# Optimization experiments

Measured on AMD Instinct MI355X. Metric: run time of the kernel, lower is better.

The kernel has to match this reference:

```python
import jax, jax.numpy as jnp
import numpy as np

_CH = [(3,64),(64,64),(64,128),(128,128),(128,256),(256,256),(256,256),(256,512),(512,512),(512,512),(512,512),(512,512),(512,512)]
_RES = [32,32,16,16,8,8,8,4,4,4,2,2,2]
# (conv index, pool index applied after, or None)
_PLAN = [(0,None),(1,0),(2,None),(3,1),(4,None),(5,None),(6,2),(7,None),(8,None),(9,3),(10,None),(11,None),(12,4)]


def _bilinear(x, py, px):
    # x: [B,C,H,W]; py/px: [B,K2,H,W] float sampling coords (zero-padded outside)
    B, C, H, W = x.shape
    y0 = jnp.floor(py); x0 = jnp.floor(px)
    wy1 = (py - y0)[:, None]  # [B,1,K2,H,W]
    wx1 = (px - x0)[:, None]
    xf = x.reshape(B, C, H * W)

    def gather(yi, xi):
        valid = ((yi >= 0) & (yi < H) & (xi >= 0) & (xi < W)).astype(x.dtype)
        idx = (jnp.clip(yi, 0, H - 1) * W + jnp.clip(xi, 0, W - 1)).astype(jnp.int32)
        def gb(xb, ib, vb):
            return xb[:, ib.reshape(-1)].reshape((xb.shape[0],) + ib.shape) * vb[None]
        return jax.vmap(gb)(xf, idx, valid)  # [B,C,K2,H,W]

    g00 = gather(y0, x0); g01 = gather(y0, x0 + 1)
    g10 = gather(y0 + 1, x0); g11 = gather(y0 + 1, x0 + 1)
    return (g00 * (1 - wy1) * (1 - wx1) + g01 * (1 - wy1) * wx1
            + g10 * wy1 * (1 - wx1) + g11 * wy1 * wx1)


def _deform_conv(x, offset, w, b):
    # torchvision-style DeformConv2d, stride 1, padding 1, 3x3 kernel
    B, C, H, W = x.shape
    K = w.shape[-1]
    off = offset.reshape(B, K * K, 2, H, W)  # per kernel tap: (dy, dx)
    kk = jnp.arange(K, dtype=x.dtype) - (K // 2)
    ky = jnp.repeat(kk, K); kx = jnp.tile(kk, K)  # [K2]
    py = jnp.arange(H, dtype=x.dtype)[None, None, :, None] + ky[None, :, None, None] + off[:, :, 0]
    px = jnp.arange(W, dtype=x.dtype)[None, None, None, :] + kx[None, :, None, None] + off[:, :, 1]
    s = _bilinear(x, py, px)  # [B,C,K2,H,W]
    out = jnp.einsum('bckhw,ock->bohw', s, w.reshape(w.shape[0], C, K * K))
    return out + b[None, :, None, None]


def _bn_relu(x, g, beta):
    # training-mode BatchNorm2d (batch statistics, eps=1e-5) + ReLU
    m = jnp.mean(x, axis=(0, 2, 3), keepdims=True)
    v = jnp.mean((x - m) ** 2, axis=(0, 2, 3), keepdims=True)
    xn = (x - m) * jax.lax.rsqrt(v + 1e-5)
    return jax.nn.relu(xn * g[None, :, None, None] + beta[None, :, None, None])


def _deform_pool(x, perm, new_perm):
    # permutation-indexed 2x2 max pool: gather by perm, pool, re-permute output
    B, C, H, W = x.shape
    xp = x.reshape(B, C, H * W)[:, :, perm].reshape(B, C, H, W)
    p = xp.reshape(B, C, H // 2, 2, W // 2, 2).max(axis=(3, 5))
    return p.reshape(B, C, (H // 2) * (W // 2))[:, :, new_perm].reshape(B, C, H // 2, W // 2)


def _forward(x, offs, ws, bs, gs, betas, perms, nperms, fws, fbs):
    for ci, pi in _PLAN:
        x = _deform_conv(x, offs[ci], ws[ci], bs[ci])
        x = _bn_relu(x, gs[ci], betas[ci])
        if pi is not None:
            x = _deform_pool(x, perms[pi], nperms[pi])
    h = x.reshape(x.shape[0], -1)  # [B,512]
    h = jax.nn.relu(h @ fws[0].T + fbs[0])
    h = jax.nn.relu(h @ fws[1].T + fbs[1])
    return h @ fws[2].T + fbs[2]


def setup_inputs() -> dict:
    key = jax.random.key(0)
    ks = iter(jax.random.split(key, 128))
    B = 32
    d = {"x": jax.random.normal(next(ks), (B, 3, 32, 32), jnp.float32)}
    for i, ((ci, co), r) in enumerate(zip(_CH, _RES), 1):
        d[f"off{i}"] = jax.random.normal(next(ks), (B, 18, r, r), jnp.float32) * 0.5
        d[f"w{i}"] = jax.random.normal(next(ks), (co, ci, 3, 3), jnp.float32) * (1.0 / np.sqrt(ci * 9))
        d[f"b{i}"] = jnp.zeros((co,), jnp.float32)
        d[f"g{i}"] = jnp.ones((co,), jnp.float32)
        d[f"bb{i}"] = jnp.zeros((co,), jnp.float32)
    for i, r in enumerate([32, 16, 8, 4, 2], 1):
        d[f"perm{i}"] = jax.random.permutation(next(ks), r * r)
        d[f"nperm{i}"] = jax.random.permutation(next(ks), (r // 2) * (r // 2))
    for i, (di, do) in enumerate([(512, 4096), (4096, 4096), (4096, 100)], 1):
        d[f"fw{i}"] = jax.random.normal(next(ks), (do, di), jnp.float32) * (1.0 / np.sqrt(di))
        d[f"fb{i}"] = jnp.zeros((do,), jnp.float32)
    return d


def reference(x,
              off1, off2, off3, off4, off5, off6, off7, off8, off9, off10, off11, off12, off13,
              w1, w2, w3, w4, w5, w6, w7, w8, w9, w10, w11, w12, w13,
              b1, b2, b3, b4, b5, b6, b7, b8, b9, b10, b11, b12, b13,
              g1, g2, g3, g4, g5, g6, g7, g8, g9, g10, g11, g12, g13,
              bb1, bb2, bb3, bb4, bb5, bb6, bb7, bb8, bb9, bb10, bb11, bb12, bb13,
              perm1, perm2, perm3, perm4, perm5,
              nperm1, nperm2, nperm3, nperm4, nperm5,
              fw1, fb1, fw2, fb2, fw3, fb3):
    offs = [off1, off2, off3, off4, off5, off6, off7, off8, off9, off10, off11, off12, off13]
    ws = [w1, w2, w3, w4, w5, w6, w7, w8, w9, w10, w11, w12, w13]
    bs = [b1, b2, b3, b4, b5, b6, b7, b8, b9, b10, b11, b12, b13]
    gs = [g1, g2, g3, g4, g5, g6, g7, g8, g9, g10, g11, g12, g13]
    betas = [bb1, bb2, bb3, bb4, bb5, bb6, bb7, bb8, bb9, bb10, bb11, bb12, bb13]
    perms = [perm1, perm2, perm3, perm4, perm5]
    nperms = [nperm1, nperm2, nperm3, nperm4, nperm5]
    return _forward(x, offs, ws, bs, gs, betas, perms, nperms, [fw1, fw2, fw3], [fb1, fb2, fb3])
```

## Files before the change

kernel.cpp:

```cpp
#include <hip/hip_runtime.h>
#include <hip/hip_bf16.h>

typedef __hip_bfloat16 bf16;
typedef __attribute__((ext_vector_type(8))) short short8;
typedef __attribute__((ext_vector_type(4))) short short4v;
typedef __attribute__((ext_vector_type(4))) float f32x4;
typedef unsigned short u16;
#define BF2F(x) __bfloat162float(x)

__device__ __forceinline__ u16 f2bfbits(float v) {
  bf16 h = __float2bfloat16(v);
  return *(u16*)&h;
}
__device__ __forceinline__ float bfbits2f(u16 u) {
  bf16 h; *(u16*)&h = u;
  return BF2F(h);
}
__device__ __forceinline__ void splitbf(float v, u16& hi, u16& lo) {
  hi = f2bfbits(v);
  lo = f2bfbits(v - bfbits2f(hi));
}

union VecU {
  u16 u[8];
  short8 s;
};

__global__ void nchw2nhwc_kernel(const float* __restrict__ in, float* __restrict__ out,
                                 int B, int C, int HW) {
  int i = blockIdx.x * blockDim.x + threadIdx.x;
  int total = B * C * HW;
  if (i >= total) return;
  int c = i % C; int p = (i / C) % HW; int b = i / (C * HW);
  out[i] = in[((size_t)b * C + c) * HW + p];
}

template<int C, int Kp>
__device__ __forceinline__ void wtc_pair(const float* __restrict__ w, u16* __restrict__ Wh,
// ... 20 lines not shown
    const float* w4, const float* w5, const float* w6, const float* w7,
    const float* w8, const float* w9, const float* w10, const float* w11,
    const float* w12, u16* __restrict__ Wh, u16* __restrict__ Wl) {
  int i = blockIdx.x * blockDim.x + threadIdx.x;
  if (i >= PAIR_TOTAL + PAD_TOTAL) return;
  if (i >= PAIR_TOTAL) {
    int t = i - PAIR_TOTAL;
    int co = t / 5, k = 27 + t % 5;
    int o = co * 32 + k;
    Wh[o] = 0; Wl[o] = 0;
    return;
  }
  if      (i < 192)     wtc_pair<3, 32>(w0, Wh + 0, Wl + 0, i);
  else if (i < 4288)    wtc_pair<64, 576>(w1, Wh + 2048, Wl + 2048, i - 192);
  else if (i < 12480)   wtc_pair<64, 576>(w2, Wh + 38912, Wl + 38912, i - 4288);
  else if (i < 28864)   wtc_pair<128, 1152>(w3, Wh + 112640, Wl + 112640, i - 12480);
  else if (i < 61632)   wtc_pair<128, 1152>(w4, Wh + 260096, Wl + 260096, i - 28864);
  else if (i < 127168)  wtc_pair<256, 2304>(w5, Wh + 555008, Wl + 555008, i - 61632);
  else if (i < 192704)  wtc_pair<256, 2304>(w6, Wh + 1144832, Wl + 1144832, i - 127168);
  else if (i < 323776)  wtc_pair<256, 2304>(w7, Wh + 1734656, Wl + 1734656, i - 192704);
  else if (i < 585920)  wtc_pair<512, 4608>(w8, Wh + 2914304, Wl + 2914304, i - 323776);
  else if (i < 848064)  wtc_pair<512, 4608>(w9, Wh + 5273600, Wl + 5273600, i - 585920);
  else if (i < 1110208) wtc_pair<512, 4608>(w10, Wh + 7632896, Wl + 7632896, i - 848064);
  else if (i < 1372352) wtc_pair<512, 4608>(w11, Wh + 9992192, Wl + 9992192, i - 1110208);
  else                  wtc_pair<512, 4608>(w12, Wh + 12351488, Wl + 12351488, i - 1372352);
}

__global__ void act_convert(const float* __restrict__ x,
                            u16* __restrict__ Ah, u16* __restrict__ Al, int total) {
  int i = blockIdx.x * blockDim.x + threadIdx.x;
  if (i >= total) return;
  u16 hh, ll; splitbf(x[i], hh, ll);
  Ah[i] = hh; Al[i] = ll;
}

__global__ __launch_bounds__(256) void deform_sample_v3(
    const float* __restrict__ act, const float* __restrict__ stp, int bnmode,
    const float* __restrict__ off, u16* __restrict__ Sh, u16* __restrict__ Sl,
    int m0, int Mc, int B, int H, int W, int C, int Kp) {
  int i = blockIdx.x * blockDim.x + threadIdx.x;
  int c8n = C >> 3;
  int total = Mc * 9 * c8n;
  if (i >= total) return;
  int c8 = i % c8n;
  int t = i / c8n;
  int k2 = t % 9;
  int ml = t / 9;
  int m = m0 + ml;
  int HW = H * W;
  int b = m / HW; int p = m - b * HW; int y = p / W; int x = p - y * W;
  size_t ob = (size_t)b * 18 * HW + p;
  float dy = off[ob + (size_t)(2 * k2) * HW];
  float dx = off[ob + (size_t)(2 * k2 + 1) * HW];
  float py = (float)(y + k2 / 3 - 1) + dy;
  float px = (float)(x + k2 % 3 - 1) + dx;
  float y0f = floorf(py), x0f = floorf(px);
  float wy = py - y0f, wx = px - x0f;
  int iy0 = (int)y0f, ix0 = (int)x0f;
  int iy1 = iy0 + 1, ix1 = ix0 + 1;
  float w00 = (1.f - wy) * (1.f - wx), w01 = (1.f - wy) * wx;
  float w10 = wy * (1.f - wx), w11 = wy * wx;
  if (iy0 < 0 || iy0 >= H) { w00 = 0.f; w01 = 0.f; }
  if (iy1 < 0 || iy1 >= H) { w10 = 0.f; w11 = 0.f; }
  if (ix0 < 0 || ix0 >= W) { w00 = 0.f; w10 = 0.f; }
  if (ix1 < 0 || ix1 >= W) { w01 = 0.f; w11 = 0.f; }
  int cy0 = min(max(iy0, 0), H - 1), cy1 = min(max(iy1, 0), H - 1);
  int cx0 = min(max(ix0, 0), W - 1), cx1 = min(max(ix1, 0), W - 1);
  int c = c8 << 3;
  size_t rowb = (size_t)b * HW;
  const float* p00 = act + (rowb + cy0 * W + cx0) * C + c;
  const float* p01 = act + (rowb + cy0 * W + cx1) * C + c;
  const float* p10 = act + (rowb + cy1 * W + cx0) * C + c;
  const float* p11 = act + (rowb + cy1 * W + cx1) * C + c;
  float4 a00 = *(const float4*)p00, b00 = *(const float4*)(p00 + 4);
  float4 a01 = *(const float4*)p01, b01 = *(const float4*)(p01 + 4);
  float4 a10 = *(const float4*)p10, b10 = *(const float4*)(p10 + 4);
  float4 a11 = *(const float4*)p11, b11 = *(const float4*)(p11 + 4);
  float v00[8] = {a00.x, a00.y, a00.z, a00.w, b00.x, b00.y, b00.z, b00.w};
  float v01[8] = {a01.x, a01.y, a01.z, a01.w, b01.x, b01.y, b01.z, b01.w};
  float v10[8] = {a10.x, a10.y, a10.z, a10.w, b10.x, b10.y, b10.z, b10.w};
  float v11[8] = {a11.x, a11.y, a11.z, a11.w, b11.x, b11.y, b11.z, b11.w};
  if (bnmode) {
    float4 s0 = *(const float4*)(stp + c), s1 = *(const float4*)(stp + c + 4);
    float4 h0 = *(const float4*)(stp + 512 + c), h1 = *(const float4*)(stp + 512 + c + 4);
    float sc[8] = {s0.x, s0.y, s0.z, s0.w, s1.x, s1.y, s1.z, s1.w};
    float sh[8] = {h0.x, h0.y, h0.z, h0.w, h1.x, h1.y, h1.z, h1.w};
#pragma unroll
    for (int j = 0; j < 8; ++j) {
      v00[j] = fmaxf(v00[j] * sc[j] + sh[j], 0.f);
      v01[j] = fmaxf(v01[j] * sc[j] + sh[j], 0.f);
      v10[j] = fmaxf(v10[j] * sc[j] + sh[j], 0.f);
      v11[j] = fmaxf(v11[j] * sc[j] + sh[j], 0.f);
    }
  }
  VecU uh, ul;
#pragma unroll
  for (int j = 0; j < 8; ++j) {
    float r = w00 * v00[j] + w01 * v01[j] + w10 * v10[j] + w11 * v11[j];
    splitbf(r, uh.u[j], ul.u[j]);
  }
  size_t base = (size_t)ml * Kp + (size_t)k2 * C + c;
  *(short8*)(Sh + base) = uh.s;
  *(short8*)(Sl + base) = ul.s;
}

__global__ __launch_bounds__(256) void deform_sample_scalar(
    const float* __restrict__ act, const float* __restrict__ off,
    u16* __restrict__ Sh, u16* __restrict__ Sl,
    int m0, int Mc, int B, int H, int W, int C, int Kp) {
  int i = blockIdx.x * blockDim.x + threadIdx.x;
  int total = Mc * Kp;
  if (i >= total) return;
  int kp = i % Kp;
  int ml = i / Kp;
  float val = 0.f;
  int K = 9 * C;
  if (kp < K) {
    int c = kp % C; int k2 = kp / C;
    int m = m0 + ml;
    int HW = H * W;
    int b = m / HW; int p = m - b * HW; int y = p / W; int x = p - y * W;
    size_t ob = (size_t)b * 18 * HW + p;
    float dy = off[ob + (size_t)(2 * k2) * HW];
    float dx = off[ob + (size_t)(2 * k2 + 1) * HW];
    float py = (float)(y + k2 / 3 - 1) + dy;
    float px = (float)(x + k2 % 3 - 1) + dx;
    float y0f = floorf(py), x0f = floorf(px);
    float wy = py - y0f, wx = px - x0f;
    int iy0 = (int)y0f, ix0 = (int)x0f;
    int iy1 = iy0 + 1, ix1 = ix0 + 1;
    float w00 = (1.f - wy) * (1.f - wx), w01 = (1.f - wy) * wx;
    float w10 = wy * (1.f - wx), w11 = wy * wx;
    if (iy0 < 0 || iy0 >= H) { w00 = 0.f; w01 = 0.f; }
    if (iy1 < 0 || iy1 >= H) { w10 = 0.f; w11 = 0.f; }
    if (ix0 < 0 || ix0 >= W) { w00 = 0.f; w10 = 0.f; }
    if (ix1 < 0 || ix1 >= W) { w01 = 0.f; w11 = 0.f; }
    int cy0 = min(max(iy0, 0), H - 1), cy1 = min(max(iy1, 0), H - 1);
    int cx0 = min(max(ix0, 0), W - 1), cx1 = min(max(ix1, 0), W - 1);
    size_t rowb = (size_t)b * HW;
    float v00 = act[(rowb + cy0 * W + cx0) * C + c];
    float v01 = act[(rowb + cy0 * W + cx1) * C + c];
    float v10 = act[(rowb + cy1 * W + cx0) * C + c];
    float v11 = act[(rowb + cy1 * W + cx1) * C + c];
    val = w00 * v00 + w01 * v01 + w10 * v10 + w11 * v11;
  }
  u16 hh, ll; splitbf(val, hh, ll);
  size_t base = (size_t)ml * Kp + kp;
  Sh[base] = hh; Sl[base] = ll;
}

#define LDA 40

__global__ __launch_bounds__(256) void mfma_gemm_tiled(
    const u16* __restrict__ Ah, const u16* __restrict__ Al,
    const u16* __restrict__ Bh, const u16* __restrict__ Bl,
    float* __restrict__ Cf, int M, int N, int Kp, int kPerZ, int splitMode) {
  __shared__ __align__(16) u16 lds[2 * 4 * 64 * LDA];
  const int TS = 64 * LDA;
  const int BS = 4 * TS;
  int tid = threadIdx.x;
  int lane = tid & 63, wave = tid >> 6;
  int l15 = lane & 15, quad = lane >> 4;
  int wr = wave >> 1, wc = wave & 1;
  int m0 = blockIdx.x * 64, n0 = blockIdx.y * 64;
  int kStart = blockIdx.z * kPerZ;
  int kEnd = min(Kp, kStart + kPerZ);
  int nSteps = (kEnd - kStart) >> 5;

  int sr = tid >> 2, sc = (tid & 3) << 3;
  const u16* gAh = Ah + (size_t)(m0 + sr) * Kp + kStart + sc;
  const u16* gAl = Al + (size_t)(m0 + sr) * Kp + kStart + sc;
  const u16* gBh = Bh + (size_t)(n0 + sr) * Kp + kStart + sc;
  const u16* gBl = Bl + (size_t)(n0 + sr) * Kp + kStart + sc;
  int soff = sr * LDA + sc;

  f32x4 z4 = {0.f, 0.f, 0.f, 0.f};
  f32x4 acc00 = z4, acc01 = z4, acc10 = z4, acc11 = z4;

  {
    short8 a = *(const short8*)gAh;
    short8 b = *(const short8*)gAl;
    short8 c = *(const short8*)gBh;
    short8 d = *(const short8*)gBl;
    *(short8*)&lds[0 * TS + soff] = a;
    *(short8*)&lds[1 * TS + soff] = b;
    *(short8*)&lds[2 * TS + soff] = c;
    *(short8*)&lds[3 * TS + soff] = d;
  }
  __syncthreads();

  int raoff = (wr * 32 + l15) * LDA + quad * 8;
  int rboff = (wc * 32 + l15) * LDA + quad * 8;

  for (int i = 0; i < nSteps; ++i) {
    int cb = (i & 1) * BS;
    bool hasNext = (i + 1 < nSteps);
    short8 nA, nB, nC, nD;
    if (hasNext) {
      int kn = (i + 1) << 5;
      nA = *(const short8*)(gAh + kn);
      nB = *(const short8*)(gAl + kn);
      nC = *(const short8*)(gBh + kn);
      nD = *(const short8*)(gBl + kn);
    }
    short8 ah0 = *(const short8*)&lds[cb + 0 * TS + raoff];
    short8 ah1 = *(const short8*)&lds[cb + 0 * TS + raoff + 16 * LDA];
    short8 al0 = *(const short8*)&lds[cb + 1 * TS + raoff];
    short8 al1 = *(const short8*)&lds[cb + 1 * TS + raoff + 16 * LDA];
    short8 bh0 = *(const short8*)&lds[cb + 2 * TS + rboff];
    short8 bh1 = *(const short8*)&lds[cb + 2 * TS + rboff + 16 * LDA];
    short8 bl0 = *(const short8*)&lds[cb + 3 * TS + rboff];
    short8 bl1 = *(const short8*)&lds[cb + 3 * TS + rboff + 16 * LDA];
    acc00 = __builtin_amdgcn_mfma_f32_16x16x32_bf16(ah0, bh0, acc00, 0, 0, 0);
    acc01 = __builtin_amdgcn_mfma_f32_16x16x32_bf16(ah0, bh1, acc01, 0, 0, 0);
    acc10 = __builtin_amdgcn_mfma_f32_16x16x32_bf16(ah1, bh0, acc10, 0, 0, 0);
    acc11 = __builtin_amdgcn_mfma_f32_16x16x32_bf16(ah1, bh1, acc11, 0, 0, 0);
    acc00 = __builtin_amdgcn_mfma_f32_16x16x32_bf16(ah0, bl0, acc00, 0, 0, 0);
    acc01 = __builtin_amdgcn_mfma_f32_16x16x32_bf16(ah0, bl1, acc01, 0, 0, 0);
    acc10 = __builtin_amdgcn_mfma_f32_16x16x32_bf16(ah1, bl0, acc10, 0, 0, 0);
    acc11 = __builtin_amdgcn_mfma_f32_16x16x32_bf16(ah1, bl1, acc11, 0, 0, 0);
    acc00 = __builtin_amdgcn_mfma_f32_16x16x32_bf16(al0, bh0, acc00, 0, 0, 0);
    acc01 = __builtin_amdgcn_mfma_f32_16x16x32_bf16(al0, bh1, acc01, 0, 0, 0);
    acc10 = __builtin_amdgcn_mfma_f32_16x16x32_bf16(al1, bh0, acc10, 0, 0, 0);
    acc11 = __builtin_amdgcn_mfma_f32_16x16x32_bf16(al1, bh1, acc11, 0, 0, 0);
    if (hasNext) {
      int ob = cb ^ BS;
      *(short8*)&lds[ob + 0 * TS + soff] = nA;
      *(short8*)&lds[ob + 1 * TS + soff] = nB;
      *(short8*)&lds[ob + 2 * TS + soff] = nC;
      *(short8*)&lds[ob + 3 * TS + soff] = nD;
      __syncthreads();
    }
  }

  float* out = Cf + (splitMode ? (size_t)blockIdx.z * M * N : (size_t)0);
  f32x4 av[2][2] = {{acc00, acc01}, {acc10, acc11}};
#pragma unroll
  for (int t = 0; t < 2; ++t) {
    int mB = m0 + wr * 32 + t * 16 + (quad << 2);
#pragma unroll
    for (int u = 0; u < 2; ++u) {
      int n = n0 + wc * 32 + u * 16 + l15;
      f32x4 a = av[t][u];
#pragma unroll
      for (int reg = 0; reg < 4; ++reg) {
        int m = mB + reg;
        out[(size_t)m * N + n] = a[reg];
      }
    }
  }
}

#define LDAF 40

__global__ __launch_bounds__(256) void mfma_gemm_fc4(
    const u16* __restrict__ Ah, const u16* __restrict__ Al,
    const float* __restrict__ Bw, float* __restrict__ Cf,
    int N, int K, int kPerZ) {
  __shared__ __align__(16) u16 sB[2][2][64 * LDAF];
  int tid = threadIdx.x;
  int lane = tid & 63, wave = tid >> 6;
  int l15 = lane & 15, quad = lane >> 4;
  int wm = wave >> 1, wn = wave & 1;
  int n0 = blockIdx.y * 64;
  int kStart = blockIdx.z * kPerZ;
  int kEnd = min(K, kStart + kPerZ);
  int nSteps = (kEnd - kStart) >> 5;

  int sr = tid >> 2, sc = (tid & 3) << 3;
  int gn = n0 + sr; if (gn >= N) gn = 0;
  const float* gB = Bw + (size_t)gn * K + kStart + sc;
  int soff = sr * LDAF + sc;

  const u16* pa = Ah + (size_t)(wm * 16 + l15) * K + kStart + (quad << 3);
  const u16* qa = Al + (size_t)(wm * 16 + l15) * K + kStart + (quad << 3);

  f32x4 z4 = {0.f, 0.f, 0.f, 0.f};
  f32x4 acc0 = z4, acc1 = z4;

  {
    float4 x0 = *(const float4*)gB;
    float4 x1 = *(const float4*)(gB + 4);
    float f[8] = {x0.x, x0.y, x0.z, x0.w, x1.x, x1.y, x1.z, x1.w};
    VecU uh, ul;
#pragma unroll
// ... 44 lines not shown
#pragma unroll
  for (int u = 0; u < 2; ++u) {
    int n = n0 + wn * 32 + u * 16 + l15;
    if (n >= N) continue;
    f32x4 a = av[u];
#pragma unroll
    for (int reg = 0; reg < 4; ++reg) {
      int m = wm * 16 + (quad << 2) + reg;
      out[(size_t)m * N + n] = a[reg];
    }
  }
}

__global__ void fc_reduce_convert(const float* __restrict__ P, const float* __restrict__ bias,
                                  u16* __restrict__ Ah, u16* __restrict__ Al,
                                  int MN, int N, int zs) {
  int i = blockIdx.x * blockDim.x + threadIdx.x;
  if (i >= MN) return;
  float s = 0.f;
  for (int z = 0; z < zs; ++z) s += P[(size_t)z * MN + i];
  s += bias[i % N];
  if (s < 0.f) s = 0.f;
  u16 hh, ll; splitbf(s, hh, ll);
  Ah[i] = hh; Al[i] = ll;
}

__global__ void fc_reduce_out(const float* __restrict__ P, const float* __restrict__ bias,
                              float* __restrict__ out, int MN, int N, int zs) {
  int i = blockIdx.x * blockDim.x + threadIdx.x;
  if (i >= MN) return;
  float s = 0.f;
  for (int z = 0; z < zs; ++z) s += P[(size_t)z * MN + i];
  out[i] = s + bias[i % N];
}

__global__ void zreduce_kernel(const float* __restrict__ P, float* __restrict__ out,
                               int MN, int zs) {
  int i = blockIdx.x * blockDim.x + threadIdx.x;
  if (i >= MN) return;
  float s = 0.f;
  for (int z = 0; z < zs; ++z) s += P[(size_t)z * MN + i];
  out[i] = s;
}

__global__ __launch_bounds__(256) void bn_stats_fused(
    const float* __restrict__ P, float* __restrict__ out, float* __restrict__ st,
    const float* __restrict__ g, const float* __restrict__ bb,
    int M, int C, int rowsPerBlock, int nBlocks, int zs, int writeOut) {
  __shared__ float sh[512];
  __shared__ int isLast;
  size_t MN = (size_t)M * C;
  int t = threadIdx.x;
  int r0 = blockIdx.x * rowsPerBlock;
  int r1 = min(M, r0 + rowsPerBlock);
  if (C >= 256) {
    for (int c = t; c < C; c += 256) {
      float s = 0.f, ss = 0.f;
      for (int r = r0; r < r1; ++r) {
        size_t idx = (size_t)r * C + c;
        float v = P[idx];
        for (int z = 1; z < zs; ++z) v += P[(size_t)z * MN + idx];
        if (writeOut) out[idx] = v;
        s += v; ss += v * v;
      }
      atomicAdd(&st[c], s); atomicAdd(&st[512 + c], ss);
    }
  } else {
    int rpb = 256 / C;
    int c = t % C; int ro = t / C;
    float s = 0.f, ss = 0.f;
    for (int r = r0 + ro; r < r1; r += rpb) {
      size_t idx = (size_t)r * C + c;
      float v = P[idx];
      for (int z = 1; z < zs; ++z) v += P[(size_t)z * MN + idx];
      if (writeOut) out[idx] = v;
// ... 43 lines not shown
#pragma unroll
  for (int dy = 0; dy < 2; ++dy)
#pragma unroll
    for (int dx = 0; dx < 2; ++dx) {
      int p = min(max(perm[(2 * qy + dy) * H + (2 * qx + dx)], 0), HW - 1);
      float v = in[((size_t)b * HW + p) * C + c];
      v = fmaxf(v * sc + sh, 0.f);
      m = fmaxf(m, v);
    }
  out[((size_t)b * oHW + j) * C + c] = m;
}

static inline void pick_split4(int gx, int gy, int Kp, int& zs, int& kPerZ) {
  int gxy = gx * gy;
  zs = 1;
  if (gxy < 512) {
    zs = (512 + gxy - 1) / gxy;
    int maxz = Kp / 32; if (maxz < 1) maxz = 1;
    if (zs > maxz) zs = maxz;
  }
  kPerZ = (((Kp + zs - 1) / zs) + 31) & ~31;
  zs = (Kp + kPerZ - 1) / kPerZ;
}

static inline void pick_splitFC(int gy, int K, int& zs, int& kPerZ) {
  zs = (512 + gy - 1) / gy;
  int maxz = K / 32; if (maxz < 1) maxz = 1;
  if (zs > maxz) zs = maxz;
  if (zs > 32) zs = 32;
  kPerZ = (((K + zs - 1) / zs) + 31) & ~31;
  zs = (K + kPerZ - 1) / kPerZ;
}

extern "C" void kernel_launch(void* const* d_in, const int* in_sizes, int n_in,
                              void* d_out, int out_size, void* d_ws, size_t ws_size,
                              hipStream_t stream) {
  const int Ci[13]  = {3, 64, 64, 128, 128, 256, 256, 256, 512, 512, 512, 512, 512};
  const int CoA[13] = {64, 64, 128, 128, 256, 256, 256, 512, 512, 512, 512, 512, 512};
  const int Rr[13]  = {32, 32, 16, 16, 8, 8, 8, 4, 4, 4, 2, 2, 2};
  const int poolAfter[13] = {-1, 0, -1, 1, -1, -1, 2, -1, -1, 3, -1, -1, 4};
  const size_t wOff[13] = {0, 2048, 38912, 112640, 260096, 555008, 1144832, 1734656,
                           2914304, 5273600, 7632896, 9992192, 12351488};
  const int WT_TOTAL = 14710784;
  const int B = 32;
  const int ST = 2304;

  size_t cursor = 0;
  auto alloc = [&](size_t bytes) {
    void* p = (char*)d_ws + cursor;
    cursor += (bytes + 255) & ~(size_t)255;
    return p;
  };
  float* stats = (float*)alloc((size_t)13 * ST * 4);
  u16*   fcPh  = (u16*)alloc((size_t)32 * 4096 * 2);
  u16*   fcPl  = (u16*)alloc((size_t)32 * 4096 * 2);
  float* A0    = (float*)alloc((size_t)2097152 * 4);
  float* A1    = (float*)alloc((size_t)2097152 * 4);
  u16*   WTh   = (u16*)alloc((size_t)WT_TOTAL * 2);
  u16*   WTl   = (u16*)alloc((size_t)WT_TOTAL * 2);
  float* Pbuf  = (float*)alloc((size_t)4194304 * 4);
  size_t remainBytes = (ws_size > cursor) ? (ws_size - cursor) : 0;
  size_t sElems = remainBytes / 4;
  if (sElems > (size_t)20971520) sElems = 20971520;
  if (sElems < (size_t)589824)  sElems = 589824;
  u16* Sh = (u16*)alloc(sElems * 2);
  u16* Sl = (u16*)alloc(sElems * 2);
  (void)in_sizes; (void)n_in; (void)out_size;

  hipMemsetAsync(stats, 0, (size_t)13 * ST * 4, stream);

  {
    int total = B * 3 * 1024;
    nchw2nhwc_kernel<<<(total + 255) / 256, 256, 0, stream>>>(
        (const float*)d_in[0], A0, B, 3, 1024);
  }
  wtc_all_v2<<<(PAIR_TOTAL + PAD_TOTAL + 255) / 256, 256, 0, stream>>>(
      (const float*)d_in[2],  (const float*)d_in[7],  (const float*)d_in[12],
      (const float*)d_in[17], (const float*)d_in[22], (const float*)d_in[27],
      (const float*)d_in[32], (const float*)d_in[37], (const float*)d_in[42],
      (const float*)d_in[47], (const float*)d_in[52], (const float*)d_in[57],
      (const float*)d_in[62], WTh, WTl);

  float* cur = A0;
  float* oth = A1;
  int needBN = 0;
  float* stp = nullptr;

  for (int l = 0; l < 13; ++l) {
    int C = Ci[l], N = CoA[l], H = Rr[l];
    int M = B * H * H, K = 9 * C, Kp = (K + 31) & ~31;
    const float* offp = (const float*)d_in[1 + l * 5 + 0];
    const float* gp   = (const float*)d_in[1 + l * 5 + 3];
    const float* bbp  = (const float*)d_in[1 + l * 5 + 4];
    float* st = stats + (size_t)l * ST;

    int MC = (int)((sElems / (size_t)Kp) & ~(size_t)63);
    if (MC < 64) MC = 64;
    if (MC > M) MC = M;
    bool singleChunk = (MC >= M);
    int lastZs = 1;
    for (int r0 = 0; r0 < M; r0 += MC) {
      int Mc = min(MC, M - r0);
      if ((C & 7) == 0) {
        int work = Mc * 9 * (C >> 3);
        deform_sample_v3<<<(work + 255) / 256, 256, 0, stream>>>(
            cur, stp, needBN, offp, Sh, Sl, r0, Mc, B, H, H, C, Kp);
      } else {
        int work = Mc * Kp;
        deform_sample_scalar<<<(work + 255) / 256, 256, 0, stream>>>(
            cur, offp, Sh, Sl, r0, Mc, B, H, H, C, Kp);
      }
      int gx = Mc / 64, gy = N / 64;
      int zs, kPerZ;
      pick_split4(gx, gy, Kp, zs, kPerZ);
      lastZs = zs;
      float* gemmOut = (zs > 1) ? Pbuf : (oth + (size_t)r0 * N);
      mfma_gemm_tiled<<<dim3(gx, gy, zs), 256, 0, stream>>>(
          Sh, Sl, WTh + wOff[l], WTl + wOff[l], gemmOut, Mc, N, Kp, kPerZ, zs > 1 ? 1 : 0);
      if (zs > 1 && !singleChunk)
        zreduce_kernel<<<(Mc * N + 255) / 256, 256, 0, stream>>>(
            Pbuf, oth + (size_t)r0 * N, Mc * N, zs);
    }

    int rowsPer = M / 128;
    if (rowsPer < 1) rowsPer = 1;
    if (rowsPer > 64) rowsPer = 64;
    int nB = (M + rowsPer - 1) / rowsPer;
    if (singleChunk && lastZs > 1)
      bn_stats_fused<<<nB, 256, 0, stream>>>(Pbuf, oth, st, gp, bbp,
                                             M, N, rowsPer, nB, lastZs, 1);
    else
      bn_stats_fused<<<nB, 256, 0, stream>>>(oth, oth, st, gp, bbp,
                                             M, N, rowsPer, nB, 1, 0);

    if (poolAfter[l] >= 0) {
      int pi = poolAfter[l];
      const int* perm  = (const int*)d_in[66 + pi * 2];
      const int* nperm = (const int*)d_in[66 + pi * 2 + 1];
      int oH = H / 2;
      int total = B * oH * oH * N;
      pool_kernel<<<(total + 255) / 256, 256, 0, stream>>>(oth, st + 1024, cur,
                                                           perm, nperm, B, H, N, total);
      needBN = 0; stp = nullptr;
    } else {
      float* t = cur; cur = oth; oth = t;
      needBN = 1; stp = st + 1024;
    }
  }

  const float* fw1 = (const float*)d_in[76]; const float* fb1 = (const float*)d_in[77];
  const float* fw2 = (const float*)d_in[78]; const float* fb2 = (const float*)d_in[79];
  const float* fw3 = (const float*)d_in[80]; const float* fb3 = (const float*)d_in[81];
  {
    int zs, kPerZ;
    act_convert<<<(32 * 512 + 255) / 256, 256, 0, stream>>>(cur, fcPh, fcPl, 32 * 512);
    pick_splitFC(64, 512, zs, kPerZ);
    mfma_gemm_fc4<<<dim3(1, 64, zs), 256, 0, stream>>>(fcPh, fcPl, fw1, Pbuf,
                                                       4096, 512, kPerZ);
    fc_reduce_convert<<<(32 * 4096 + 255) / 256, 256, 0, stream>>>(
        Pbuf, fb1, fcPh, fcPl, 32 * 4096, 4096, zs);
    pick_splitFC(64, 4096, zs, kPerZ);
    mfma_gemm_fc4<<<dim3(1, 64, zs), 256, 0, stream>>>(fcPh, fcPl, fw2, Pbuf,
                                                       4096, 4096, kPerZ);
// ... 10 lines not shown
```

Measured before the change: 907.5 us.

## Widen split-bf16 MFMA GEMM tile from 64x64 to 64x128 along N

The GEMM block now covers 128 output columns instead of 64, so each wave computes a 32x64 sub-tile with eight accumulators. Each A fragment loaded from LDS is reused across four B fragments, which cuts LDS and global traffic on A per MFMA. The grid in N is halved (rounded up) and the split-K partial buffer is doubled, presumably so pick_split4 can choose more K splits to make up for fewer blocks. The cost is more registers per thread and a larger LDS footprint, which may lower occupancy. For layers with N=64, half of each tile's B loads read past the layer's weight rows; those results are masked on store but are wasted work.

```diff
diff --git a/kernel.cpp b/kernel.cpp
--- a/kernel.cpp
+++ b/kernel.cpp
@@ -213,93 +213,98 @@
     const u16* __restrict__ Ah, const u16* __restrict__ Al,
     const u16* __restrict__ Bh, const u16* __restrict__ Bl,
     float* __restrict__ Cf, int M, int N, int Kp, int kPerZ, int splitMode) {
-  __shared__ __align__(16) u16 lds[2 * 4 * 64 * LDA];
-  const int TS = 64 * LDA;
-  const int BS = 4 * TS;
+  __shared__ __align__(16) u16 lds[2 * 384 * LDA];
+  const int BS = 384 * LDA;
   int tid = threadIdx.x;
   int lane = tid & 63, wave = tid >> 6;
   int l15 = lane & 15, quad = lane >> 4;
   int wr = wave >> 1, wc = wave & 1;
-  int m0 = blockIdx.x * 64, n0 = blockIdx.y * 64;
+  int m0 = blockIdx.x * 64, n0 = blockIdx.y * 128;
   int kStart = blockIdx.z * kPerZ;
   int kEnd = min(Kp, kStart + kPerZ);
   int nSteps = (kEnd - kStart) >> 5;
 
   int sr = tid >> 2, sc = (tid & 3) << 3;
-  const u16* gAh = Ah + (size_t)(m0 + sr) * Kp + kStart + sc;
-  const u16* gAl = Al + (size_t)(m0 + sr) * Kp + kStart + sc;
-  const u16* gBh = Bh + (size_t)(n0 + sr) * Kp + kStart + sc;
-  const u16* gBl = Bl + (size_t)(n0 + sr) * Kp + kStart + sc;
-  int soff = sr * LDA + sc;
+  const u16* g0 = Ah + (size_t)(m0 + sr) * Kp + kStart + sc;
+  const u16* g1 = Al + (size_t)(m0 + sr) * Kp + kStart + sc;
+  const u16* g2 = Bh + (size_t)(n0 + sr) * Kp + kStart + sc;
+  const u16* g3 = Bh + (size_t)(n0 + 64 + sr) * Kp + kStart + sc;
+  const u16* g4 = Bl + (size_t)(n0 + sr) * Kp + kStart + sc;
+  const u16* g5 = Bl + (size_t)(n0 + 64 + sr) * Kp + kStart + sc;
+  int s0 = (0 * 64 + sr) * LDA + sc;
+  int s1 = (1 * 64 + sr) * LDA + sc;
+  int s2 = (2 * 64 + sr) * LDA + sc;
+  int s3 = (3 * 64 + sr) * LDA + sc;
+  int s4 = (4 * 64 + sr) * LDA + sc;
+  int s5 = (5 * 64 + sr) * LDA + sc;
 
   f32x4 z4 = {0.f, 0.f, 0.f, 0.f};
-  f32x4 acc00 = z4, acc01 = z4, acc10 = z4, acc11 = z4;
+  f32x4 acc[2][4];
+#pragma unroll
+  for (int t = 0; t < 2; ++t)
+#pragma unroll
+    for (int u = 0; u < 4; ++u) acc[t][u] = z4;
 
   {
-    short8 a = *(const short8*)gAh;
-    short8 b = *(const short8*)gAl;
-    short8 c = *(const short8*)gBh;
-    short8 d = *(const short8*)gBl;
-    *(short8*)&lds[0 * TS + soff] = a;
-    *(short8*)&lds[1 * TS + soff] = b;
-    *(short8*)&lds[2 * TS + soff] = c;
-    *(short8*)&lds[3 * TS + soff] = d;
+    short8 r0 = *(const short8*)g0, r1 = *(const short8*)g1;
+    short8 r2 = *(const short8*)g2, r3 = *(const short8*)g3;
+    short8 r4 = *(const short8*)g4, r5 = *(const short8*)g5;
+    *(short8*)&lds[s0] = r0; *(short8*)&lds[s1] = r1;
+    *(short8*)&lds[s2] = r2; *(short8*)&lds[s3] = r3;
+    *(short8*)&lds[s4] = r4; *(short8*)&lds[s5] = r5;
   }
   __syncthreads();
 
   int raoff = (wr * 32 + l15) * LDA + quad * 8;
-  int rboff = (wc * 32 + l15) * LDA + quad * 8;
+  int rboff = (128 + wc * 64 + l15) * LDA + quad * 8;
 
   for (int i = 0; i < nSteps; ++i) {
     int cb = (i & 1) * BS;
     bool hasNext = (i + 1 < nSteps);
-    short8 nA, nB, nC, nD;
+    short8 n0r, n1r, n2r, n3r, n4r, n5r;
     if (hasNext) {
       int kn = (i + 1) << 5;
-      nA = *(const short8*)(gAh + kn);
-      nB = *(const short8*)(gAl + kn);
-      nC = *(const short8*)(gBh + kn);
-      nD = *(const short8*)(gBl + kn);
-    }
-    short8 ah0 = *(const short8*)&lds[cb + 0 * TS + raoff];
-    short8 ah1 = *(const short8*)&lds[cb + 0 * TS + raoff + 16 * LDA];
-    short8 al0 = *(const short8*)&lds[cb + 1 * TS + raoff];
-    short8 al1 = *(const short8*)&lds[cb + 1 * TS + raoff + 16 * LDA];
-    short8 bh0 = *(const short8*)&lds[cb + 2 * TS + rboff];
-    short8 bh1 = *(const short8*)&lds[cb + 2 * TS + rboff + 16 * LDA];
-    short8 bl0 = *(const short8*)&lds[cb + 3 * TS + rboff];
-    short8 bl1 = *(const short8*)&lds[cb + 3 * TS + rboff + 16 * LDA];
-    acc00 = __builtin_amdgcn_mfma_f32_16x16x32_bf16(ah0, bh0, acc00, 0, 0, 0);
-    acc01 = __builtin_amdgcn_mfma_f32_16x16x32_bf16(ah0, bh1, acc01, 0, 0, 0);
-    acc10 = __builtin_amdgcn_mfma_f32_16x16x32_bf16(ah1, bh0, acc10, 0, 0, 0);
-    acc11 = __builtin_amdgcn_mfma_f32_16x16x32_bf16(ah1, bh1, acc11, 0, 0, 0);
-    acc00 = __builtin_amdgcn_mfma_f32_16x16x32_bf16(ah0, bl0, acc00, 0, 0, 0);
-    acc01 = __builtin_amdgcn_mfma_f32_16x16x32_bf16(ah0, bl1, acc01, 0, 0, 0);
-    acc10 = __builtin_amdgcn_mfma_f32_16x16x32_bf16(ah1, bl0, acc10, 0, 0, 0);
-    acc11 = __builtin_amdgcn_mfma_f32_16x16x32_bf16(ah1, bl1, acc11, 0, 0, 0);
-    acc00 = __builtin_amdgcn_mfma_f32_16x16x32_bf16(al0, bh0, acc00, 0, 0, 0);
-    acc01 = __builtin_amdgcn_mfma_f32_16x16x32_bf16(al0, bh1, acc01, 0, 0, 0);
-    acc10 = __builtin_amdgcn_mfma_f32_16x16x32_bf16(al1, bh0, acc10, 0, 0, 0);
-    acc11 = __builtin_amdgcn_mfma_f32_16x16x32_bf16(al1, bh1, acc11, 0, 0, 0);
+      n0r = *(const short8*)(g0 + kn); n1r = *(const short8*)(g1 + kn);
+      n2r = *(const short8*)(g2 + kn); n3r = *(const short8*)(g3 + kn);
+      n4r = *(const short8*)(g4 + kn); n5r = *(const short8*)(g5 + kn);
+    }
+    short8 ah0 = *(const short8*)&lds[cb + raoff];
+    short8 ah1 = *(const short8*)&lds[cb + raoff + 16 * LDA];
+    short8 al0 = *(const short8*)&lds[cb + raoff + 64 * LDA];
+    short8 al1 = *(const short8*)&lds[cb + raoff + 80 * LDA];
+    short8 bh[4], bl[4];
+#pragma unroll
+    for (int u = 0; u < 4; ++u) {
+      bh[u] = *(const short8*)&lds[cb + rboff + u * 16 * LDA];
+      bl[u] = *(const short8*)&lds[cb + rboff + (128 + u * 16) * LDA];
+    }
+#pragma unroll
+    for (int u = 0; u < 4; ++u) {
+      acc[0][u] = __builtin_amdgcn_mfma_f32_16x16x32_bf16(ah0, bh[u], acc[0][u], 0, 0, 0);
+      acc[1][u] = __builtin_amdgcn_mfma_f32_16x16x32_bf16(ah1, bh[u], acc[1][u], 0, 0, 0);
+      acc[0][u] = __builtin_amdgcn_mfma_f32_16x16x32_bf16(ah0, bl[u], acc[0][u], 0, 0, 0);
+      acc[1][u] = __builtin_amdgcn_mfma_f32_16x16x32_bf16(ah1, bl[u], acc[1][u], 0, 0, 0);
+      acc[0][u] = __builtin_amdgcn_mfma_f32_16x16x32_bf16(al0, bh[u], acc[0][u], 0, 0, 0);
+      acc[1][u] = __builtin_amdgcn_mfma_f32_16x16x32_bf16(al1, bh[u], acc[1][u], 0, 0, 0);
+    }
     if (hasNext) {
       int ob = cb ^ BS;
-      *(short8*)&lds[ob + 0 * TS + soff] = nA;
-      *(short8*)&lds[ob + 1 * TS + soff] = nB;
-      *(short8*)&lds[ob + 2 * TS + soff] = nC;
-      *(short8*)&lds[ob + 3 * TS + soff] = nD;
+      *(short8*)&lds[ob + s0] = n0r; *(short8*)&lds[ob + s1] = n1r;
+      *(short8*)&lds[ob + s2] = n2r; *(short8*)&lds[ob + s3] = n3r;
+      *(short8*)&lds[ob + s4] = n4r; *(short8*)&lds[ob + s5] = n5r;
       __syncthreads();
     }
   }
 
   float* out = Cf + (splitMode ? (size_t)blockIdx.z * M * N : (size_t)0);
-  f32x4 av[2][2] = {{acc00, acc01}, {acc10, acc11}};
 #pragma unroll
   for (int t = 0; t < 2; ++t) {
     int mB = m0 + wr * 32 + t * 16 + (quad << 2);
 #pragma unroll
-    for (int u = 0; u < 2; ++u) {
-      int n = n0 + wc * 32 + u * 16 + l15;
-      f32x4 a = av[t][u];
+    for (int u = 0; u < 4; ++u) {
+      int n = n0 + wc * 64 + u * 16 + l15;
+      if (n >= N) continue;
+      f32x4 a = acc[t][u];
 #pragma unroll
       for (int reg = 0; reg < 4; ++reg) {
         int m = mB + reg;
@@ -563,7 +568,7 @@
   float* A1    = (float*)alloc((size_t)2097152 * 4);
   u16*   WTh   = (u16*)alloc((size_t)WT_TOTAL * 2);
   u16*   WTl   = (u16*)alloc((size_t)WT_TOTAL * 2);
-  float* Pbuf  = (float*)alloc((size_t)4194304 * 4);
+  float* Pbuf  = (float*)alloc((size_t)8388608 * 4);
   size_t remainBytes = (ws_size > cursor) ? (ws_size - cursor) : 0;
   size_t sElems = remainBytes / 4;
   if (sElems > (size_t)20971520) sElems = 20971520;
@@ -615,7 +620,7 @@
         deform_sample_scalar<<<(work + 255) / 256, 256, 0, stream>>>(
             cur, offp, Sh, Sl, r0, Mc, B, H, H, C, Kp);
       }
-      int gx = Mc / 64, gy = N / 64;
+      int gx = Mc / 64, gy = (N + 127) / 128;
       int zs, kPerZ;
       pick_split4(gx, gy, Kp, zs, kPerZ);
       lastZs = zs;
```

Measured after the change: 1.045 ms. 15.2% more time.

## Fuse deformable bilinear sampling into the MFMA GEMM A-tile loader

Applied to the files above, without the earlier changes.

Layers after the first no longer materialize the sampled im2col matrix in a workspace buffer. Each GEMM block instead computes the bilinear samples (with optional BN+ReLU) on the fly while loading its A tile into shared memory, double-buffered against the MFMA work. The goal is to remove the large Sh/Sl global write and read traffic and the chunking and z-reduce launches. In exchange, sampling is recomputed once per N-tile column of blocks, and the kernel assumes power-of-two H, W and C for its bit-mask indexing.

```diff
diff --git a/kernel.cpp b/kernel.cpp
--- a/kernel.cpp
+++ b/kernel.cpp
@@ -3,7 +3,6 @@
 
 typedef __hip_bfloat16 bf16;
 typedef __attribute__((ext_vector_type(8))) short short8;
-typedef __attribute__((ext_vector_type(4))) short short4v;
 typedef __attribute__((ext_vector_type(4))) float f32x4;
 typedef unsigned short u16;
 #define BF2F(x) __bfloat162float(x)
@@ -90,76 +89,6 @@
   if (i >= total) return;
   u16 hh, ll; splitbf(x[i], hh, ll);
   Ah[i] = hh; Al[i] = ll;
-}
-
-__global__ __launch_bounds__(256) void deform_sample_v3(
-    const float* __restrict__ act, const float* __restrict__ stp, int bnmode,
-    const float* __restrict__ off, u16* __restrict__ Sh, u16* __restrict__ Sl,
-    int m0, int Mc, int B, int H, int W, int C, int Kp) {
-  int i = blockIdx.x * blockDim.x + threadIdx.x;
-  int c8n = C >> 3;
-  int total = Mc * 9 * c8n;
-  if (i >= total) return;
-  int c8 = i % c8n;
-  int t = i / c8n;
-  int k2 = t % 9;
-  int ml = t / 9;
-  int m = m0 + ml;
-  int HW = H * W;
-  int b = m / HW; int p = m - b * HW; int y = p / W; int x = p - y * W;
-  size_t ob = (size_t)b * 18 * HW + p;
-  float dy = off[ob + (size_t)(2 * k2) * HW];
-  float dx = off[ob + (size_t)(2 * k2 + 1) * HW];
-  float py = (float)(y + k2 / 3 - 1) + dy;
-  float px = (float)(x + k2 % 3 - 1) + dx;
-  float y0f = floorf(py), x0f = floorf(px);
-  float wy = py - y0f, wx = px - x0f;
-  int iy0 = (int)y0f, ix0 = (int)x0f;
-  int iy1 = iy0 + 1, ix1 = ix0 + 1;
-  float w00 = (1.f - wy) * (1.f - wx), w01 = (1.f - wy) * wx;
-  float w10 = wy * (1.f - wx), w11 = wy * wx;
-  if (iy0 < 0 || iy0 >= H) { w00 = 0.f; w01 = 0.f; }
-  if (iy1 < 0 || iy1 >= H) { w10 = 0.f; w11 = 0.f; }
-  if (ix0 < 0 || ix0 >= W) { w00 = 0.f; w10 = 0.f; }
-  if (ix1 < 0 || ix1 >= W) { w01 = 0.f; w11 = 0.f; }
-  int cy0 = min(max(iy0, 0), H - 1), cy1 = min(max(iy1, 0), H - 1);
-  int cx0 = min(max(ix0, 0), W - 1), cx1 = min(max(ix1, 0), W - 1);
-  int c = c8 << 3;
-  size_t rowb = (size_t)b * HW;
-  const float* p00 = act + (rowb + cy0 * W + cx0) * C + c;
-  const float* p01 = act + (rowb + cy0 * W + cx1) * C + c;
-  const float* p10 = act + (rowb + cy1 * W + cx0) * C + c;
-  const float* p11 = act + (rowb + cy1 * W + cx1) * C + c;
-  float4 a00 = *(const float4*)p00, b00 = *(const float4*)(p00 + 4);
-  float4 a01 = *(const float4*)p01, b01 = *(const float4*)(p01 + 4);
-  float4 a10 = *(const float4*)p10, b10 = *(const float4*)(p10 + 4);
-  float4 a11 = *(const float4*)p11, b11 = *(const float4*)(p11 + 4);
-  float v00[8] = {a00.x, a00.y, a00.z, a00.w, b00.x, b00.y, b00.z, b00.w};
-  float v01[8] = {a01.x, a01.y, a01.z, a01.w, b01.x, b01.y, b01.z, b01.w};
-  float v10[8] = {a10.x, a10.y, a10.z, a10.w, b10.x, b10.y, b10.z, b10.w};
-  float v11[8] = {a11.x, a11.y, a11.z, a11.w, b11.x, b11.y, b11.z, b11.w};
-  if (bnmode) {
-    float4 s0 = *(const float4*)(stp + c), s1 = *(const float4*)(stp + c + 4);
-    float4 h0 = *(const float4*)(stp + 512 + c), h1 = *(const float4*)(stp + 512 + c + 4);
-    float sc[8] = {s0.x, s0.y, s0.z, s0.w, s1.x, s1.y, s1.z, s1.w};
-    float sh[8] = {h0.x, h0.y, h0.z, h0.w, h1.x, h1.y, h1.z, h1.w};
-#pragma unroll
-    for (int j = 0; j < 8; ++j) {
-      v00[j] = fmaxf(v00[j] * sc[j] + sh[j], 0.f);
-      v01[j] = fmaxf(v01[j] * sc[j] + sh[j], 0.f);
-      v10[j] = fmaxf(v10[j] * sc[j] + sh[j], 0.f);
-      v11[j] = fmaxf(v11[j] * sc[j] + sh[j], 0.f);
-    }
-  }
-  VecU uh, ul;
-#pragma unroll
-  for (int j = 0; j < 8; ++j) {
-    float r = w00 * v00[j] + w01 * v01[j] + w10 * v10[j] + w11 * v11[j];
-    splitbf(r, uh.u[j], ul.u[j]);
-  }
-  size_t base = (size_t)ml * Kp + (size_t)k2 * C + c;
-  *(short8*)(Sh + base) = uh.s;
-  *(short8*)(Sl + base) = ul.s;
 }
 
 __global__ __launch_bounds__(256) void deform_sample_scalar(
@@ -309,6 +238,163 @@
   }
 }
 
+__global__ __launch_bounds__(256) void mfma_gemm_fused(
+    const float* __restrict__ act, const float* __restrict__ stp, int bnmode,
+    const float* __restrict__ off,
+    const u16* __restrict__ Bh, const u16* __restrict__ Bl,
+    float* __restrict__ Cf, int M, int N, int Kp, int kPerZ, int splitMode,
+    int H, int W, int C, int lc, int lhw, int lw) {
+  __shared__ __align__(16) u16 lds[2 * 4 * 64 * LDA];
+  const int TS = 64 * LDA;
+  const int BS = 4 * TS;
+  int tid = threadIdx.x;
+  int lane = tid & 63, wave = tid >> 6;
+  int l15 = lane & 15, quad = lane >> 4;
+  int wr = wave >> 1, wc = wave & 1;
+  int m0 = blockIdx.x * 64, n0 = blockIdx.y * 64;
+  int kStart = blockIdx.z * kPerZ;
+  int kEnd = min(Kp, kStart + kPerZ);
+  int nSteps = (kEnd - kStart) >> 5;
+
+  int sr = tid >> 2, sc = (tid & 3) << 3;
+  int HWv = H * W;
+  int m = m0 + sr;
+  int b = m >> lhw; int p = m & (HWv - 1); int y = p >> lw; int x = p & (W - 1);
+  size_t obase = (size_t)b * 18 * HWv + p;
+  size_t rowb = (size_t)b * HWv;
+  const u16* gBh = Bh + (size_t)(n0 + sr) * Kp + kStart + sc;
+  const u16* gBl = Bl + (size_t)(n0 + sr) * Kp + kStart + sc;
+  int soff = sr * LDA + sc;
+
+  f32x4 z4 = {0.f, 0.f, 0.f, 0.f};
+  f32x4 acc00 = z4, acc01 = z4, acc10 = z4, acc11 = z4;
+
+  auto SAMPLE = [&](int kk, short8& uh8, short8& ul8) {
+    int k2 = kk >> lc;
+    int ci = kk & (C - 1);
+    float dy = off[obase + (size_t)(2 * k2) * HWv];
+    float dx = off[obase + (size_t)(2 * k2 + 1) * HWv];
+    float py = (float)(y + k2 / 3 - 1) + dy;
+    float px = (float)(x + k2 % 3 - 1) + dx;
+    float y0f = floorf(py), x0f = floorf(px);
+    float wy = py - y0f, wx = px - x0f;
+    int iy0 = (int)y0f, ix0 = (int)x0f;
+    int iy1 = iy0 + 1, ix1 = ix0 + 1;
+    float w00 = (1.f - wy) * (1.f - wx), w01 = (1.f - wy) * wx;
+    float w10 = wy * (1.f - wx), w11 = wy * wx;
+    if (iy0 < 0 || iy0 >= H) { w00 = 0.f; w01 = 0.f; }
+    if (iy1 < 0 || iy1 >= H) { w10 = 0.f; w11 = 0.f; }
+    if (ix0 < 0 || ix0 >= W) { w00 = 0.f; w10 = 0.f; }
+    if (ix1 < 0 || ix1 >= W) { w01 = 0.f; w11 = 0.f; }
+    int cy0 = min(max(iy0, 0), H - 1), cy1 = min(max(iy1, 0), H - 1);
+    int cx0 = min(max(ix0, 0), W - 1), cx1 = min(max(ix1, 0), W - 1);
+    const float* p00 = act + (rowb + cy0 * W + cx0) * C + ci;
+    const float* p01 = act + (rowb + cy0 * W + cx1) * C + ci;
+    const float* p10 = act + (rowb + cy1 * W + cx0) * C + ci;
+    const float* p11 = act + (rowb + cy1 * W + cx1) * C + ci;
+    float4 a00 = *(const float4*)p00, b00 = *(const float4*)(p00 + 4);
+    float4 a01 = *(const float4*)p01, b01 = *(const float4*)(p01 + 4);
+    float4 a10 = *(const float4*)p10, b10 = *(const float4*)(p10 + 4);
+    float4 a11 = *(const float4*)p11, b11 = *(const float4*)(p11 + 4);
+    float v00[8] = {a00.x, a00.y, a00.z, a00.w, b00.x, b00.y, b00.z, b00.w};
+    float v01[8] = {a01.x, a01.y, a01.z, a01.w, b01.x, b01.y, b01.z, b01.w};
+    float v10[8] = {a10.x, a10.y, a10.z, a10.w, b10.x, b10.y, b10.z, b10.w};
+    float v11[8] = {a11.x, a11.y, a11.z, a11.w, b11.x, b11.y, b11.z, b11.w};
+    if (bnmode) {
+      float4 s0 = *(const float4*)(stp + ci), s1 = *(const float4*)(stp + ci + 4);
+      float4 h0 = *(const float4*)(stp + 512 + ci), h1 = *(const float4*)(stp + 512 + ci + 4);
+      float scv[8] = {s0.x, s0.y, s0.z, s0.w, s1.x, s1.y, s1.z, s1.w};
+      float shv[8] = {h0.x, h0.y, h0.z, h0.w, h1.x, h1.y, h1.z, h1.w};
+#pragma unroll
+      for (int j = 0; j < 8; ++j) {
+        v00[j] = fmaxf(v00[j] * scv[j] + shv[j], 0.f);
+        v01[j] = fmaxf(v01[j] * scv[j] + shv[j], 0.f);
+        v10[j] = fmaxf(v10[j] * scv[j] + shv[j], 0.f);
+        v11[j] = fmaxf(v11[j] * scv[j] + shv[j], 0.f);
+      }
+    }
+    VecU uh, ul;
+#pragma unroll
+    for (int j = 0; j < 8; ++j) {
+      float r = w00 * v00[j] + w01 * v01[j] + w10 * v10[j] + w11 * v11[j];
+      splitbf(r, uh.u[j], ul.u[j]);
+    }
+    uh8 = uh.s; ul8 = ul.s;
+  };
+
+  {
+    short8 sa, sb;
+    SAMPLE(kStart + sc, sa, sb);
+    short8 c = *(const short8*)gBh;
+    short8 d = *(const short8*)gBl;
+    *(short8*)&lds[0 * TS + soff] = sa;
+    *(short8*)&lds[1 * TS + soff] = sb;
+    *(short8*)&lds[2 * TS + soff] = c;
+    *(short8*)&lds[3 * TS + soff] = d;
+  }
+  __syncthreads();
+
+  int raoff = (wr * 32 + l15) * LDA + quad * 8;
+  int rboff = (wc * 32 + l15) * LDA + quad * 8;
+
+  for (int i = 0; i < nSteps; ++i) {
+    int cb = (i & 1) * BS;
+    bool hasNext = (i + 1 < nSteps);
+    short8 nA, nB, nC, nD;
+    if (hasNext) {
+      int kn = (i + 1) << 5;
+      SAMPLE(kStart + kn + sc, nA, nB);
+      nC = *(const short8*)(gBh + kn);
+      nD = *(const short8*)(gBl + kn);
+    }
+    short8 ah0 = *(const short8*)&lds[cb + 0 * TS + raoff];
+    short8 ah1 = *(const short8*)&lds[cb + 0 * TS + raoff + 16 * LDA];
+    short8 al0 = *(const short8*)&lds[cb + 1 * TS + raoff];
+    short8 al1 = *(const short8*)&lds[cb + 1 * TS + raoff + 16 * LDA];
+    short8 bh0 = *(const short8*)&lds[cb + 2 * TS + rboff];
+    short8 bh1 = *(const short8*)&lds[cb + 2 * TS + rboff + 16 * LDA];
+    short8 bl0 = *(const short8*)&lds[cb + 3 * TS + rboff];
+    short8 bl1 = *(const short8*)&lds[cb + 3 * TS + rboff + 16 * LDA];
+    acc00 = __builtin_amdgcn_mfma_f32_16x16x32_bf16(ah0, bh0, acc00, 0, 0, 0);
+    acc01 = __builtin_amdgcn_mfma_f32_16x16x32_bf16(ah0, bh1, acc01, 0, 0, 0);
+    acc10 = __builtin_amdgcn_mfma_f32_16x16x32_bf16(ah1, bh0, acc10, 0, 0, 0);
+    acc11 = __builtin_amdgcn_mfma_f32_16x16x32_bf16(ah1, bh1, acc11, 0, 0, 0);
+    acc00 = __builtin_amdgcn_mfma_f32_16x16x32_bf16(ah0, bl0, acc00, 0, 0, 0);
+    acc01 = __builtin_amdgcn_mfma_f32_16x16x32_bf16(ah0, bl1, acc01, 0, 0, 0);
+    acc10 = __builtin_amdgcn_mfma_f32_16x16x32_bf16(ah1, bl0, acc10, 0, 0, 0);
+    acc11 = __builtin_amdgcn_mfma_f32_16x16x32_bf16(ah1, bl1, acc11, 0, 0, 0);
+    acc00 = __builtin_amdgcn_mfma_f32_16x16x32_bf16(al0, bh0, acc00, 0, 0, 0);
+    acc01 = __builtin_amdgcn_mfma_f32_16x16x32_bf16(al0, bh1, acc01, 0, 0, 0);
+    acc10 = __builtin_amdgcn_mfma_f32_16x16x32_bf16(al1, bh0, acc10, 0, 0, 0);
+    acc11 = __builtin_amdgcn_mfma_f32_16x16x32_bf16(al1, bh1, acc11, 0, 0, 0);
+    if (hasNext) {
+      int ob = cb ^ BS;
+      *(short8*)&lds[ob + 0 * TS + soff] = nA;
+      *(short8*)&lds[ob + 1 * TS + soff] = nB;
+      *(short8*)&lds[ob + 2 * TS + soff] = nC;
+      *(short8*)&lds[ob + 3 * TS + soff] = nD;
+      __syncthreads();
+    }
+  }
+
+  float* out = Cf + (splitMode ? (size_t)blockIdx.z * M * N : (size_t)0);
+  f32x4 av[2][2] = {{acc00, acc01}, {acc10, acc11}};
+#pragma unroll
+  for (int t = 0; t < 2; ++t) {
+    int mB = m0 + wr * 32 + t * 16 + (quad << 2);
+#pragma unroll
+    for (int u = 0; u < 2; ++u) {
+      int n = n0 + wc * 32 + u * 16 + l15;
+      f32x4 a = av[t][u];
+#pragma unroll
+      for (int reg = 0; reg < 4; ++reg) {
+        int mm = mB + reg;
+        out[(size_t)mm * N + n] = a[reg];
+      }
+    }
+  }
+}
+
 #define LDAF 40
 
 __global__ __launch_bounds__(256) void mfma_gemm_fc4(
@@ -419,15 +505,6 @@
   float s = 0.f;
   for (int z = 0; z < zs; ++z) s += P[(size_t)z * MN + i];
   out[i] = s + bias[i % N];
-}
-
-__global__ void zreduce_kernel(const float* __restrict__ P, float* __restrict__ out,
-                               int MN, int zs) {
-  int i = blockIdx.x * blockDim.x + threadIdx.x;
-  if (i >= MN) return;
-  float s = 0.f;
-  for (int z = 0; z < zs; ++z) s += P[(size_t)z * MN + i];
-  out[i] = s;
 }
 
 __global__ __launch_bounds__(256) void bn_stats_fused(
@@ -537,6 +614,8 @@
   zs = (K + kPerZ - 1) / kPerZ;
 }
 
+static inline int ilog2(int v) { int l = 0; while ((1 << l) < v) ++l; return l; }
+
 extern "C" void kernel_launch(void* const* d_in, const int* in_sizes, int n_in,
                               void* d_out, int out_size, void* d_ws, size_t ws_size,
                               hipStream_t stream) {
@@ -564,12 +643,8 @@
   u16*   WTh   = (u16*)alloc((size_t)WT_TOTAL * 2);
   u16*   WTl   = (u16*)alloc((size_t)WT_TOTAL * 2);
   float* Pbuf  = (float*)alloc((size_t)4194304 * 4);
-  size_t remainBytes = (ws_size > cursor) ? (ws_size - cursor) : 0;
-  size_t sElems = remainBytes / 4;
-  if (sElems > (size_t)20971520) sElems = 20971520;
-  if (sElems < (size_t)589824)  sElems = 589824;
-  u16* Sh = (u16*)alloc(sElems * 2);
-  u16* Sl = (u16*)alloc(sElems * 2);
+  u16*   Sh    = (u16*)alloc((size_t)1048576 * 2);
+  u16*   Sl    = (u16*)alloc((size_t)1048576 * 2);
   (void)in_sizes; (void)n_in; (void)out_size;
 
   hipMemsetAsync(stats, 0, (size_t)13 * ST * 4, stream);
@@ -599,41 +674,31 @@
     const float* bbp  = (const float*)d_in[1 + l * 5 + 4];
     float* st = stats + (size_t)l * ST;
 
-    int MC = (int)((sElems / (size_t)Kp) & ~(size_t)63);
-    if (MC < 64) MC = 64;
-    if (MC > M) MC = M;
-    bool singleChunk = (MC >= M);
-    int lastZs = 1;
-    for (int r0 = 0; r0 < M; r0 += MC) {
-      int Mc = min(MC, M - r0);
-      if ((C & 7) == 0) {
-        int work = Mc * 9 * (C >> 3);
-        deform_sample_v3<<<(work + 255) / 256, 256, 0, stream>>>(
-            cur, stp, needBN, offp, Sh, Sl, r0, Mc, B, H, H, C, Kp);
-      } else {
-        int work = Mc * Kp;
-        deform_sample_scalar<<<(work + 255) / 256, 256, 0, stream>>>(
-            cur, offp, Sh, Sl, r0, Mc, B, H, H, C, Kp);
-      }
-      int gx = Mc / 64, gy = N / 64;
-      int zs, kPerZ;
-      pick_split4(gx, gy, Kp, zs, kPerZ);
-      lastZs = zs;
-      float* gemmOut = (zs > 1) ? Pbuf : (oth + (size_t)r0 * N);
+    int gx = M / 64, gy = N / 64;
+    int zs, kPerZ;
+    pick_split4(gx, gy, Kp, zs, kPerZ);
+    float* gemmOut = (zs > 1) ? Pbuf : oth;
+
+    if (l == 0) {
+      int work = M * Kp;
+      deform_sample_scalar<<<(work + 255) / 256, 256, 0, stream>>>(
+          cur, offp, Sh, Sl, 0, M, B, H, H, C, Kp);
       mfma_gemm_tiled<<<dim3(gx, gy, zs), 256, 0, stream>>>(
-          Sh, Sl, WTh + wOff[l], WTl + wOff[l], gemmOut, Mc, N, Kp, kPerZ, zs > 1 ? 1 : 0);
-      if (zs > 1 && !singleChunk)
-        zreduce_kernel<<<(Mc * N + 255) / 256, 256, 0, stream>>>(
-            Pbuf, oth + (size_t)r0 * N, Mc * N, zs);
+          Sh, Sl, WTh + wOff[l], WTl + wOff[l], gemmOut, M, N, Kp, kPerZ, zs > 1 ? 1 : 0);
+    } else {
+      int lw_ = ilog2(H), lhw_ = 2 * lw_, lc_ = ilog2(C);
+      mfma_gemm_fused<<<dim3(gx, gy, zs), 256, 0, stream>>>(
+          cur, stp, needBN, offp, WTh + wOff[l], WTl + wOff[l],
+          gemmOut, M, N, Kp, kPerZ, zs > 1 ? 1 : 0, H, H, C, lc_, lhw_, lw_);
     }
 
     int rowsPer = M / 128;
     if (rowsPer < 1) rowsPer = 1;
     if (rowsPer > 64) rowsPer = 64;
     int nB = (M + rowsPer - 1) / rowsPer;
-    if (singleChunk && lastZs > 1)
+    if (zs > 1)
       bn_stats_fused<<<nB, 256, 0, stream>>>(Pbuf, oth, st, gp, bbp,
-                                             M, N, rowsPer, nB, lastZs, 1);
+                                             M, N, rowsPer, nB, zs, 1);
     else
       bn_stats_fused<<<nB, 256, 0, stream>>>(oth, oth, st, gp, bbp,
                                              M, N, rowsPer, nB, 1, 0);
```

Measured after the change: 958.9 us. +5.7%, slower.
